# Performance work log

Measured on AMD Instinct MI355X. Metric: run time of the kernel, lower is better.

The kernel has to match this reference:

```python
import jax, jax.numpy as jnp
import numpy as np

N = 100000          # nodes
E = 1_600_000       # edges (before self loops)
IN = 128            # in_channels
HID = 64            # hidden
HEADS = 4
EPS = 1e-5          # BatchNorm eps
NEG_SLOPE = 0.2     # GATConv leaky_relu slope


def setup_inputs() -> dict:
    key = jax.random.key(0)
    ks = jax.random.split(key, 16)
    he = lambda fan: (2.0 / fan) ** 0.5  # kaiming-normal scale
    d = {
        "x": jax.random.normal(ks[0], (N, IN), jnp.float32),
        "edge_index": jax.random.randint(ks[1], (2, E), 0, N, dtype=jnp.int64),
        "root_index": 0,
        "W1": jax.random.normal(ks[2], (IN, HEADS * HID), jnp.float32) * he(IN),
        "att_src1": jax.random.normal(ks[3], (HEADS, HID), jnp.float32) * 0.1,
        "att_dst1": jax.random.normal(ks[4], (HEADS, HID), jnp.float32) * 0.1,
        "b1": jnp.zeros((HEADS * HID,), jnp.float32),
        "W2": jax.random.normal(ks[5], (HEADS * HID, HID), jnp.float32) * he(HEADS * HID),
        "att_src2": jax.random.normal(ks[6], (1, HID), jnp.float32) * 0.1,
        "att_dst2": jax.random.normal(ks[7], (1, HID), jnp.float32) * 0.1,
        "b2": jnp.zeros((HID,), jnp.float32),
        "bn1_g": jnp.ones((HEADS * HID,), jnp.float32),
        "bn1_b": jnp.zeros((HEADS * HID,), jnp.float32),
        "bn1_m": jnp.zeros((HEADS * HID,), jnp.float32),
        "bn1_v": jnp.ones((HEADS * HID,), jnp.float32),
        "bn2_g": jnp.ones((HID,), jnp.float32),
        "bn2_b": jnp.zeros((HID,), jnp.float32),
        "bn2_m": jnp.zeros((HID,), jnp.float32),
        "bn2_v": jnp.ones((HID,), jnp.float32),
        "cg1_w": jax.random.normal(ks[8], (3 * HID, 64), jnp.float32) * he(3 * HID),
        "cg1_b": jnp.zeros((64,), jnp.float32),
        "cbn_g": jnp.ones((64,), jnp.float32),
        "cbn_b": jnp.zeros((64,), jnp.float32),
        "cbn_m": jnp.zeros((64,), jnp.float32),
        "cbn_v": jnp.ones((64,), jnp.float32),
        "cg2_w": jax.random.normal(ks[9], (64, 32), jnp.float32) * he(64),
        "cg2_b": jnp.zeros((32,), jnp.float32),
        "cg3_w": jax.random.normal(ks[10], (32, 1), jnp.float32) * he(32),
        "cg3_b": jnp.zeros((1,), jnp.float32),
    }
    return d


def _bn_eval(x, g, b, m, v):
    return (x - m) * jax.lax.rsqrt(v + EPS) * g + b


def _gat_conv(x, src, dst, W, att_src, att_dst, bias, heads, out_ch, concat):
    """PyG GATConv (eval mode, self loops already in src/dst)."""
    n = x.shape[0]
    h = (x @ W).reshape(n, heads, out_ch)                # [N,H,C]
    a_src = jnp.einsum('nhc,hc->nh', h, att_src)         # [N,H]
    a_dst = jnp.einsum('nhc,hc->nh', h, att_dst)
    e = jax.nn.leaky_relu(a_src[src] + a_dst[dst], NEG_SLOPE)   # [Etot,H]
    seg_max = jax.ops.segment_max(e, dst, num_segments=n)
    ex = jnp.exp(e - seg_max[dst])
    denom = jax.ops.segment_sum(ex, dst, num_segments=n)
    alpha = ex / (denom[dst] + 1e-16)                    # [Etot,H]
    msg = h[src] * alpha[:, :, None]                     # [Etot,H,C]
    out = jax.ops.segment_sum(msg, dst, num_segments=n)  # [N,H,C]
    if concat:
        return out.reshape(n, heads * out_ch) + bias
    return out.mean(axis=1) + bias


def reference(x, edge_index, root_index, W1, att_src1, att_dst1, b1,
              W2, att_src2, att_dst2, b2,
              bn1_g, bn1_b, bn1_m, bn1_v, bn2_g, bn2_b, bn2_m, bn2_v,
              cg1_w, cg1_b, cbn_g, cbn_b, cbn_m, cbn_v,
              cg2_w, cg2_b, cg3_w, cg3_b):
    n = x.shape[0]
    # add self loops (PyG GATConv default)
    loop = jnp.arange(n, dtype=edge_index.dtype)
    src = jnp.concatenate([edge_index[0], loop])
    dst = jnp.concatenate([edge_index[1], loop])

    h = _gat_conv(x, src, dst, W1, att_src1, att_dst1, b1, HEADS, HID, True)
    h = jax.nn.elu(_bn_eval(h, bn1_g, bn1_b, bn1_m, bn1_v))
    h = _gat_conv(h, src, dst, W2, att_src2, att_dst2, b2, 1, HID, False)
    node_emb = jax.nn.elu(_bn_eval(h, bn2_g, bn2_b, bn2_m, bn2_v))  # [N,HID]

    mean_emb = node_emb.mean(axis=0, keepdims=True)      # [1,HID]
    max_emb = node_emb.max(axis=0, keepdims=True)        # [1,HID]
    safe_root = min(root_index, n - 1)
    root_emb = node_emb[safe_root][None, :]              # single graph path
    g = jnp.concatenate([mean_emb, max_emb, root_emb], axis=-1)  # [1,3*HID]

    g = jax.nn.relu(_bn_eval(g @ cg1_w + cg1_b, cbn_g, cbn_b, cbn_m, cbn_v))
    g = jax.nn.relu(g @ cg2_w + cg2_b)
    logit = (g @ cg3_w + cg3_b).squeeze(-1)              # [1]
    return logit
```

## Files before the change

### kernel.cpp

```cpp
#include <hip/hip_runtime.h>

#define N_NODES 100000
#define N_EDGES 1600000
#define ETOT    1700000
#define IN_CH   128
#define C1      256
#define HID     64
#define BN_EPS  1e-5f
#define SLOPE   0.2f
#define NCHUNK  98
#define DEG_PH  8
#define DEG_PHN 12500
#define FILL_PH 12
#define FILL_PHN 8334

typedef __attribute__((ext_vector_type(8))) short s16x8;
typedef __attribute__((ext_vector_type(4))) float f32x4;
#define MFMA16(a, b, c) __builtin_amdgcn_mfma_f32_16x16x32_bf16(a, b, c, 0, 0, 0)

__device__ __forceinline__ float leaky(float x) { return fmaxf(x, SLOPE * x); }
__device__ __forceinline__ float elu_f(float x) { return x > 0.f ? x : __expf(x) - 1.f; }
__device__ __forceinline__ unsigned short f2bf(float f) {
  unsigned int b = __float_as_uint(f);
  return (unsigned short)((b + 0x7FFFu + ((b >> 16) & 1u)) >> 16);
}
__device__ __forceinline__ float bf2f(unsigned short u) {
  return __uint_as_float((unsigned int)u << 16);
}
__device__ __forceinline__ unsigned int encf(float f) {
  unsigned int b = __float_as_uint(f);
  return b ^ ((((int)b >> 31)) | 0x80000000u);
}
__device__ __forceinline__ float decf(unsigned int k) {
  unsigned int b = (k & 0x80000000u) ? (k ^ 0x80000000u) : ~k;
  return __uint_as_float(b);
}

__global__ void __launch_bounds__(256) k_prep_init(const float* __restrict__ W1, const float* __restrict__ W2,
                                                   unsigned short* __restrict__ W1T, unsigned short* __restrict__ W2T,
                                                   int* __restrict__ deg, float* __restrict__ psum,
                                                   unsigned int* __restrict__ pmaxenc) {
  int i = blockIdx.x * 256 + threadIdx.x;
  if (i < N_NODES) deg[i] = 1;
  if (i < IN_CH * C1) {
    int k = i >> 8, c = i & 255;
    W1T[c * IN_CH + k] = f2bf(W1[i]);
  }
  if (i < C1 * HID) {
    int k = i >> 6, c = i & 63;
    W2T[c * C1 + k] = f2bf(W2[i]);
  }
  if (i < 256 * 64) { psum[i] = 0.f; pmaxenc[i] = 0u; }
}

__global__ void __launch_bounds__(256) k_deg_ph(const int* __restrict__ edge, int* __restrict__ deg) {
  int bpp = (N_EDGES + 1023) >> 10;
  int ph = blockIdx.x / bpp;
  int lo = ph * DEG_PHN, hi = lo + DEG_PHN;
  int i0 = (blockIdx.x % bpp) * 1024 + threadIdx.x * 4;
  if (i0 >= N_EDGES) return;
  if (i0 + 3 < N_EDGES) {
    int4 dv = *(const int4*)(edge + N_EDGES + i0);
    if (dv.x >= lo && dv.x < hi) atomicAdd(&deg[dv.x], 1);
    if (dv.y >= lo && dv.y < hi) atomicAdd(&deg[dv.y], 1);
    if (dv.z >= lo && dv.z < hi) atomicAdd(&deg[dv.z], 1);
    if (dv.w >= lo && dv.w < hi) atomicAdd(&deg[dv.w], 1);
  } else {
    for (int j = 0; j < 4 && i0 + j < N_EDGES; j++) {
      int d = edge[N_EDGES + i0 + j];
      if (d >= lo && d < hi) atomicAdd(&deg[d], 1);
    }
  }
}

__global__ void __launch_bounds__(256) k_scan_part(const int* __restrict__ deg, int* __restrict__ part) {
  __shared__ int ls[256];
  int t = threadIdx.x;
  int base = blockIdx.x * 1024 + t * 4;
  int s = 0;
#pragma unroll
  for (int j = 0; j < 4; j++) if (base + j < N_NODES) s += deg[base + j];
  ls[t] = s;
  __syncthreads();
  for (int off = 128; off >= 1; off >>= 1) {
    if (t < off) ls[t] += ls[t + off];
    __syncthreads();
  }
  if (t == 0) part[blockIdx.x] = ls[0];
}

__global__ void k_scan_top(int* __restrict__ part, int* __restrict__ row_ptr) {
  if (threadIdx.x == 0 && blockIdx.x == 0) {
    int run = 0;
    for (int i = 0; i < NCHUNK; i++) { int t = part[i]; part[i] = run; run += t; }
    row_ptr[N_NODES] = run;
  }
}

__global__ void __launch_bounds__(256) k_scan_down(const int* __restrict__ deg, const int* __restrict__ part,
                                                   int* __restrict__ row_ptr, int* __restrict__ cursor) {
  __shared__ int ls[256];
  int t = threadIdx.x;
  int base = blockIdx.x * 1024 + t * 4;
  int v[4];
#pragma unroll
  for (int j = 0; j < 4; j++) v[j] = (base + j < N_NODES) ? deg[base + j] : 0;
  int tsum = v[0] + v[1] + v[2] + v[3];
  ls[t] = tsum;
  __syncthreads();
  for (int off = 1; off < 256; off <<= 1) {
    int add = (t >= off) ? ls[t - off] : 0;
    __syncthreads();
    ls[t] += add;
    __syncthreads();
  }
  int excl = ls[t] - tsum + part[blockIdx.x];
#pragma unroll
  for (int j = 0; j < 4; j++) {
    int idx = base + j;
    if (idx < N_NODES) { row_ptr[idx] = excl; cursor[idx] = excl; }
    excl += v[j];
  }
}

__global__ void __launch_bounds__(256) k_fill_ph(const int* __restrict__ edge, int* __restrict__ cursor,
                                                 const float* __restrict__ aS, const float* __restrict__ aD,
                                                 int* __restrict__ col, float* __restrict__ w1) {
  int bpp = (ETOT + 255) >> 8;
  int ph = blockIdx.x / bpp;
  int lo = ph * FILL_PHN, hi = lo + FILL_PHN;
  int i = (blockIdx.x % bpp) * 256 + threadIdx.x;
  if (i >= ETOT) return;
  int d = (i < N_EDGES) ? edge[N_EDGES + i] : (i - N_EDGES);
  if (d < lo || d >= hi) return;
  int s = (i < N_EDGES) ? edge[i] : d;
  int pos = atomicAdd(&cursor[d], 1);
  col[pos] = s;
  float4 as4 = *(const float4*)(aS + (size_t)s * 4);
  float4 ad4 = *(const float4*)(aD + (size_t)d * 4);
  float4 w;
  w.x = __expf(fminf(leaky(as4.x + ad4.x), 80.f));
  w.y = __expf(fminf(leaky(as4.y + ad4.y), 80.f));
  w.z = __expf(fminf(leaky(as4.z + ad4.z), 80.f));
  w.w = __expf(fminf(leaky(as4.w + ad4.w), 80.f));
  *(float4*)(w1 + (size_t)pos * 4) = w;
}

__global__ void __launch_bounds__(256) k_gemm1(const float* __restrict__ x, const unsigned short* __restrict__ W1T,
                                               const float* __restrict__ attS, const float* __restrict__ attD,
                                               unsigned short* __restrict__ h1b, float* __restrict__ aS,
                                               float* __restrict__ aD) {
  __shared__ unsigned short As[64][IN_CH + 8];
  int tid = threadIdx.x;
  int w = tid >> 6, lane = tid & 63;
  int l15 = lane & 15, l4 = lane >> 4;
  int row0 = blockIdx.x * 64;
#pragma unroll
  for (int it = 0; it < 8; it++) {
    int idx = tid + it * 256;
    int r = idx >> 5;
    int k4 = (idx & 31) * 4;
    int gr = row0 + r; if (gr >= N_NODES) gr = N_NODES - 1;
    float4 v = *(const float4*)(x + (size_t)gr * IN_CH + k4);
    ushort4 bvec;
    bvec.x = f2bf(v.x); bvec.y = f2bf(v.y); bvec.z = f2bf(v.z); bvec.w = f2bf(v.w);
    *(ushort4*)&As[r][k4] = bvec;
  }
  __syncthreads();
  f32x4 acc[4][4];
#pragma unroll
  for (int mf = 0; mf < 4; mf++)
#pragma unroll
    for (int cf = 0; cf < 4; cf++) acc[mf][cf] = (f32x4){0.f, 0.f, 0.f, 0.f};
#pragma unroll
  for (int ks = 0; ks < 4; ks++) {
    int koff = ks * 32 + l4 * 8;
    s16x8 a[4];
#pragma unroll
    for (int mf = 0; mf < 4; mf++) a[mf] = *(const s16x8*)&As[mf * 16 + l15][koff];
#pragma unroll
    for (int cf = 0; cf < 4; cf++) {
      s16x8 b = *(const s16x8*)(W1T + (size_t)(w * 64 + cf * 16 + l15) * IN_CH + koff);
#pragma unroll
      for (int mf = 0; mf < 4; mf++) acc[mf][cf] = MFMA16(a[mf], b, acc[mf][cf]);
    }
  }
  float as_c[4], ad_c[4];
#pragma unroll
  for (int cf = 0; cf < 4; cf++) {
    as_c[cf] = attS[w * HID + cf * 16 + l15];
    ad_c[cf] = attD[w * HID + cf * 16 + l15];
  }
#pragma unroll
  for (int mf = 0; mf < 4; mf++) {
#pragma unroll
    for (int reg = 0; reg < 4; reg++) {
      int gr = row0 + mf * 16 + l4 * 4 + reg;
      bool ok = gr < N_NODES;
      float s = 0.f, dd = 0.f;
#pragma unroll
      for (int cf = 0; cf < 4; cf++) {
        float v = acc[mf][cf][reg];
        if (ok) h1b[(size_t)gr * C1 + w * 64 + cf * 16 + l15] = f2bf(v);
        s += v * as_c[cf];
        dd += v * ad_c[cf];
      }
#pragma unroll
      for (int m = 1; m <= 8; m <<= 1) { s += __shfl_xor(s, m, 64); dd += __shfl_xor(dd, m, 64); }
      if (ok && l15 == 0) {
        aS[(size_t)gr * 4 + w] = s;
        aD[(size_t)gr * 4 + w] = dd;
      }
    }
  }
}

__global__ void __launch_bounds__(1024) k_agg1g2(const int* __restrict__ row_ptr, const int* __restrict__ col,
                                                 const float* __restrict__ w1,
                                                 const unsigned short* __restrict__ h1b, const float* __restrict__ b1,
                                                 const float* __restrict__ g1, const float* __restrict__ be1,
                                                 const float* __restrict__ m1, const float* __restrict__ v1,
                                                 const unsigned short* __restrict__ W2T,
                                                 const float* __restrict__ attS2, const float* __restrict__ attD2,
                                                 unsigned short* __restrict__ h2b, float* __restrict__ aS2,
                                                 float* __restrict__ aD2) {
  __shared__ unsigned short Hm[16][C1 + 8];
  int wave = threadIdx.x >> 6;
  int lane = threadIdx.x & 63;
  int l15 = lane & 15, l4 = lane >> 4;
  int d = blockIdx.x * 16 + wave;
  int head = lane >> 4;
  int s0 = row_ptr[d], s1 = row_ptr[d + 1];
  int s1m1 = s1 - 1;
  float denom = 0.f;
  float4 acc = {0.f, 0.f, 0.f, 0.f};
  int c0 = lane * 4;
  for (int base = s0; base < s1; base += 8) {
    int left = s1 - base;
    int idx = base + (lane & 7); if (idx > s1m1) idx = s1m1;
    int cv = col[idx];
    int sid[8];
#pragma unroll
    for (int j = 0; j < 8; j++) sid[j] = __builtin_amdgcn_readfirstlane(__shfl(cv, j));
    float wv[8];
#pragma unroll
    for (int j = 0; j < 8; j++) {
      int wi = base + j; if (wi > s1m1) wi = s1m1;
      float wl = w1[(size_t)wi * 4 + head];
      wv[j] = (j < left) ? wl : 0.f;
    }
    ushort4 h[8];
#pragma unroll
    for (int j = 0; j < 8; j++) h[j] = *(const ushort4*)(h1b + ((size_t)sid[j] << 8) + c0);
#pragma unroll
    for (int j = 0; j < 8; j++) {
      denom += wv[j];
      acc.x += wv[j] * bf2f(h[j].x);
      acc.y += wv[j] * bf2f(h[j].y);
      acc.z += wv[j] * bf2f(h[j].z);
      acc.w += wv[j] * bf2f(h[j].w);
    }
  }
  float inv = 1.f / (denom + 1e-16f);
  float4 bb = *(const float4*)(b1 + c0);
  float4 gg = *(const float4*)(g1 + c0);
  float4 be = *(const float4*)(be1 + c0);
  float4 mm = *(const float4*)(m1 + c0);
  float4 vv = *(const float4*)(v1 + c0);
  ushort4 o;
  o.x = f2bf(elu_f((acc.x * inv + bb.x - mm.x) * rsqrtf(vv.x + BN_EPS) * gg.x + be.x));
  o.y = f2bf(elu_f((acc.y * inv + bb.y - mm.y) * rsqrtf(vv.y + BN_EPS) * gg.y + be.y));
  o.z = f2bf(elu_f((acc.z * inv + bb.z - mm.z) * rsqrtf(vv.z + BN_EPS) * gg.z + be.z));
  o.w = f2bf(elu_f((acc.w * inv + bb.w - mm.w) * rsqrtf(vv.w + BN_EPS) * gg.w + be.w));
  *(ushort4*)&Hm[wave][c0] = o;
  __syncthreads();
  if (wave == 0) {
    f32x4 acc2[4];
#pragma unroll
    for (int cf = 0; cf < 4; cf++) acc2[cf] = (f32x4){0.f, 0.f, 0.f, 0.f};
#pragma unroll
    for (int ks = 0; ks < 8; ks++) {
      int koff = ks * 32 + l4 * 8;
      s16x8 a = *(const s16x8*)&Hm[l15][koff];
#pragma unroll
      for (int cf = 0; cf < 4; cf++) {
        s16x8 b = *(const s16x8*)(W2T + (size_t)(cf * 16 + l15) * C1 + koff);
        acc2[cf] = MFMA16(a, b, acc2[cf]);
      }
    }
    float as_c[4], ad_c[4];
#pragma unroll
    for (int cf = 0; cf < 4; cf++) {
      as_c[cf] = attS2[cf * 16 + l15];
      ad_c[cf] = attD2[cf * 16 + l15];
    }
#pragma unroll
    for (int reg = 0; reg < 4; reg++) {
      int gr = blockIdx.x * 16 + l4 * 4 + reg;
      float s = 0.f, dd = 0.f;
#pragma unroll
      for (int cf = 0; cf < 4; cf++) {
        float v = acc2[cf][reg];
        h2b[(size_t)gr * HID + cf * 16 + l15] = f2bf(v);
        s += v * as_c[cf];
        dd += v * ad_c[cf];
      }
#pragma unroll
      for (int m = 1; m <= 8; m <<= 1) { s += __shfl_xor(s, m, 64); dd += __shfl_xor(dd, m, 64); }
      if (l15 == 0) { aS2[gr] = s; aD2[gr] = dd; }
    }
  }
}

__global__ void __launch_bounds__(256) k_agg2(const int* __restrict__ row_ptr, const int* __restrict__ col,
                                              const float* __restrict__ aS, const float* __restrict__ aD,
                                              const unsigned short* __restrict__ h2b, const float* __restrict__ b2,
                                              const float* __restrict__ g2, const float* __restrict__ be2,
                                              const float* __restrict__ m2, const float* __restrict__ v2,
                                              const int* __restrict__ rootp, float* __restrict__ psum,
                                              unsigned int* __restrict__ pmaxenc, float* __restrict__ root_emb) {
  __shared__ float ss[4][64], sm[4][64];
  int wave = threadIdx.x >> 6;
  int lane = threadIdx.x & 63;
  int d = blockIdx.x * 4 + wave;
  float ad = aD[d];
  int s0 = row_ptr[d], s1 = row_ptr[d + 1];
  int s1m1 = s1 - 1;
  float denom = 0.f, acc = 0.f;
  for (int base = s0; base < s1; base += 8) {
    int left = s1 - base;
    int idx = base + (lane & 7); if (idx > s1m1) idx = s1m1;
    int cv = col[idx];
    int sid[8];
#pragma unroll
    for (int j = 0; j < 8; j++) sid[j] = __builtin_amdgcn_readfirstlane(__shfl(cv, j));
    float e[8];
#pragma unroll
    for (int j = 0; j < 8; j++) e[j] = aS[sid[j]];
    unsigned short h[8];
#pragma unroll
    for (int j = 0; j < 8; j++) h[j] = h2b[((size_t)sid[j] << 6) + lane];
    float wv[8];
#pragma unroll
    for (int j = 0; j < 8; j++) {
      float wl = __expf(fminf(leaky(e[j] + ad), 80.f));
      wv[j] = (j < left) ? wl : 0.f;
    }
#pragma unroll
    for (int j = 0; j < 8; j++) {
      denom += wv[j];
      acc += wv[j] * bf2f(h[j]);
    }
  }
  float o = acc / (denom + 1e-16f) + b2[lane];
  o = (o - m2[lane]) * rsqrtf(v2[lane] + BN_EPS) * g2[lane] + be2[lane];
  o = elu_f(o);
  ss[wave][lane] = o;
  sm[wave][lane] = o;
  int root0 = rootp[0];
  if (root0 > N_NODES - 1) root0 = N_NODES - 1;
  if (root0 < 0) root0 = 0;
  if (d == root0) root_emb[lane] = o;
  __syncthreads();
  if (threadIdx.x < 64) {
    int c = threadIdx.x;
    float s4 = ss[0][c] + ss[1][c] + ss[2][c] + ss[3][c];
    float m4 = fmaxf(fmaxf(sm[0][c], sm[1][c]), fmaxf(sm[2][c], sm[3][c]));
    int slot = (blockIdx.x & 255) * 64 + c;
    atomicAdd(&psum[slot], s4);
    atomicMax(&pmaxenc[slot], encf(m4));
  }
}

__global__ void __launch_bounds__(256) k_final(const float* __restrict__ psum, const unsigned int* __restrict__ pmaxenc,
                                               const float* __restrict__ root_emb,
                                               const float* __restrict__ cg1w, const float* __restrict__ cg1b,
                                               const float* __restrict__ cbng, const float* __restrict__ cbnb,
                                               const float* __restrict__ cbnm, const float* __restrict__ cbnv,
                                               const float* __restrict__ cg2w, const float* __restrict__ cg2b,
                                               const float* __restrict__ cg3w, const float* __restrict__ cg3b,
                                               float* __restrict__ out) {
  __shared__ float ss[4][64], sm[4][64];
  __shared__ float g[192], t1[64], t2[32];
  int t = threadIdx.x;
  int c = t & 63, q = t >> 6;
  float s = 0.f, m = -INFINITY;
  for (int b = q; b < 256; b += 4) {
    s += psum[b * 64 + c];
    m = fmaxf(m, decf(pmaxenc[b * 64 + c]));
  }
  ss[q][c] = s; sm[q][c] = m;
  __syncthreads();
  if (t < 64) {
    float tot = ss[0][t] + ss[1][t] + ss[2][t] + ss[3][t];
    float mx = fmaxf(fmaxf(sm[0][t], sm[1][t]), fmaxf(sm[2][t], sm[3][t]));
    g[t] = tot / (float)N_NODES;
    g[64 + t] = mx;
    g[128 + t] = root_emb[t];
  }
  __syncthreads();
  if (t < 64) {
    float o = cg1b[t];
    for (int i = 0; i < 192; i++) o += g[i] * cg1w[i * 64 + t];
    o = (o - cbnm[t]) * rsqrtf(cbnv[t] + BN_EPS) * cbng[t] + cbnb[t];
    t1[t] = o > 0.f ? o : 0.f;
  }
  __syncthreads();
  if (t < 32) {
    float o = cg2b[t];
    for (int i = 0; i < 64; i++) o += t1[i] * cg2w[i * 32 + t];
    t2[t] = o > 0.f ? o : 0.f;
  }
  __syncthreads();
  if (t == 0) {
    float o = cg3b[0];
    for (int i = 0; i < 32; i++) o += t2[i] * cg3w[i];
    out[0] = o;
  }
}

extern "C" void kernel_launch(void* const* d_in, const int* in_sizes, int n_in,
                              void* d_out, int out_size, void* d_ws, size_t ws_size,
                              hipStream_t stream) {
  const float* x     = (const float*)d_in[0];
  const int*   edge  = (const int*)d_in[1];
  const int*   root  = (const int*)d_in[2];
  const float* W1    = (const float*)d_in[3];
  const float* attS1 = (const float*)d_in[4];
  const float* attD1 = (const float*)d_in[5];
  const float* b1    = (const float*)d_in[6];
  const float* W2    = (const float*)d_in[7];
  const float* attS2 = (const float*)d_in[8];
  const float* attD2 = (const float*)d_in[9];
  const float* b2    = (const float*)d_in[10];
  const float* bn1g  = (const float*)d_in[11];
  const float* bn1b  = (const float*)d_in[12];
  const float* bn1m  = (const float*)d_in[13];
  const float* bn1v  = (const float*)d_in[14];
  const float* bn2g  = (const float*)d_in[15];
  const float* bn2b  = (const float*)d_in[16];
  const float* bn2m  = (const float*)d_in[17];
  const float* bn2v  = (const float*)d_in[18];
  const float* cg1w  = (const float*)d_in[19];
  const float* cg1b  = (const float*)d_in[20];
  const float* cbng  = (const float*)d_in[21];
  const float* cbnb  = (const float*)d_in[22];
  const float* cbnm  = (const float*)d_in[23];
  const float* cbnv  = (const float*)d_in[24];
  const float* cg2w  = (const float*)d_in[25];
  const float* cg2b  = (const float*)d_in[26];
  const float* cg3w  = (const float*)d_in[27];
  const float* cg3b  = (const float*)d_in[28];

  char* ws = (char*)d_ws;
  size_t off = 0;
  auto carve = [&](size_t bytes) { char* p = ws + off; off += (bytes + 255) & ~(size_t)255; return p; };
  unsigned short* h1b = (unsigned short*)carve((size_t)N_NODES * C1 * 2);
  float* w1      = (float*)carve((size_t)ETOT * 4 * 4);
  unsigned short* h2b = (unsigned short*)carve((size_t)N_NODES * HID * 2);
  float* aS1     = (float*)carve((size_t)N_NODES * 4 * 4);
  float* aD1     = (float*)carve((size_t)N_NODES * 4 * 4);
  float* aS2     = (float*)carve((size_t)N_NODES * 4);
  float* aD2     = (float*)carve((size_t)N_NODES * 4);
  int*   deg     = (int*)  carve((size_t)N_NODES * 4);
  int*   row_ptr = (int*)  carve((size_t)(N_NODES + 1) * 4);
  int*   cursor  = (int*)  carve((size_t)N_NODES * 4);
  int*   col     = (int*)  carve((size_t)ETOT * 4);
  int*   part    = (int*)  carve(512);
  unsigned short* W1T = (unsigned short*)carve((size_t)IN_CH * C1 * 2);
  unsigned short* W2T = (unsigned short*)carve((size_t)C1 * HID * 2);
  float* psum    = (float*)carve(256 * 64 * 4);
  unsigned int* pmaxenc = (unsigned int*)carve(256 * 64 * 4);
  float* root_emb = (float*)carve(64 * 4);

  int bpp_deg  = (N_EDGES + 1023) >> 10;
  int bpp_fill = (ETOT + 255) >> 8;
  k_prep_init<<<(N_NODES + 255) / 256, 256, 0, stream>>>(W1, W2, W1T, W2T, deg, psum, pmaxenc);
  k_deg_ph<<<bpp_deg * DEG_PH, 256, 0, stream>>>(edge, deg);
  k_gemm1<<<(N_NODES + 63) / 64, 256, 0, stream>>>(x, W1T, attS1, attD1, h1b, aS1, aD1);
  k_scan_part<<<NCHUNK, 256, 0, stream>>>(deg, part);
  k_scan_top<<<1, 64, 0, stream>>>(part, row_ptr);
  k_scan_down<<<NCHUNK, 256, 0, stream>>>(deg, part, row_ptr, cursor);
  k_fill_ph<<<bpp_fill * FILL_PH, 256, 0, stream>>>(edge, cursor, aS1, aD1, col, w1);
  k_agg1g2<<<N_NODES / 16, 1024, 0, stream>>>(row_ptr, col, w1, h1b, b1, bn1g, bn1b, bn1m, bn1v,
                                              W2T, attS2, attD2, h2b, aS2, aD2);
  k_agg2<<<N_NODES / 4, 256, 0, stream>>>(row_ptr, col, aS2, aD2, h2b, b2, bn2g, bn2b, bn2m, bn2v,
                                          root, psum, pmaxenc, root_emb);
  k_final<<<1, 256, 0, stream>>>(psum, pmaxenc, root_emb, cg1w, cg1b, cbng, cbnb, cbnm, cbnv,
                                 cg2w, cg2b, cg3w, cg3b, (float*)d_out);
}
```

Baseline: 507.1 us.

## Split fused layer-1 aggregation and layer-2 GEMM into separate kernels

Unfuses the 1024-thread aggregation+GEMM kernel into a 256-thread aggregation kernel that writes the normalized hidden features to a new bf16 buffer and a separate 64-row-tile MFMA GEMM kernel. This removes the block-wide barrier where 15 of 16 waves idle while one wave runs the GEMM, and allows smaller blocks with better occupancy. In exchange it adds a full N×256 bf16 round trip through global memory and an extra launch. Layer-2 outputs are aliased into the now-dead h1b buffer.

Result: faster. 478.0 us, median of 2 (-5.7%).

```diff
diff --git a/kernel.cpp b/kernel.cpp
--- a/kernel.cpp
+++ b/kernel.cpp
@@ -215,20 +215,16 @@
   }
 }
 
-__global__ void __launch_bounds__(1024) k_agg1g2(const int* __restrict__ row_ptr, const int* __restrict__ col,
-                                                 const float* __restrict__ w1,
-                                                 const unsigned short* __restrict__ h1b, const float* __restrict__ b1,
-                                                 const float* __restrict__ g1, const float* __restrict__ be1,
-                                                 const float* __restrict__ m1, const float* __restrict__ v1,
-                                                 const unsigned short* __restrict__ W2T,
-                                                 const float* __restrict__ attS2, const float* __restrict__ attD2,
-                                                 unsigned short* __restrict__ h2b, float* __restrict__ aS2,
-                                                 float* __restrict__ aD2) {
-  __shared__ unsigned short Hm[16][C1 + 8];
+__global__ void __launch_bounds__(256) k_agg1(const int* __restrict__ row_ptr, const int* __restrict__ col,
+                                              const float* __restrict__ w1,
+                                              const unsigned short* __restrict__ h1b, const float* __restrict__ b1,
+                                              const float* __restrict__ g1, const float* __restrict__ be1,
+                                              const float* __restrict__ m1, const float* __restrict__ v1,
+                                              unsigned short* __restrict__ hmb) {
   int wave = threadIdx.x >> 6;
   int lane = threadIdx.x & 63;
-  int l15 = lane & 15, l4 = lane >> 4;
-  int d = blockIdx.x * 16 + wave;
+  int d = blockIdx.x * 4 + wave;
+  if (d >= N_NODES) return;
   int head = lane >> 4;
   int s0 = row_ptr[d], s1 = row_ptr[d + 1];
   int s1m1 = s1 - 1;
@@ -272,43 +268,61 @@
   o.y = f2bf(elu_f((acc.y * inv + bb.y - mm.y) * rsqrtf(vv.y + BN_EPS) * gg.y + be.y));
   o.z = f2bf(elu_f((acc.z * inv + bb.z - mm.z) * rsqrtf(vv.z + BN_EPS) * gg.z + be.z));
   o.w = f2bf(elu_f((acc.w * inv + bb.w - mm.w) * rsqrtf(vv.w + BN_EPS) * gg.w + be.w));
-  *(ushort4*)&Hm[wave][c0] = o;
-  __syncthreads();
-  if (wave == 0) {
-    f32x4 acc2[4];
-#pragma unroll
-    for (int cf = 0; cf < 4; cf++) acc2[cf] = (f32x4){0.f, 0.f, 0.f, 0.f};
-#pragma unroll
-    for (int ks = 0; ks < 8; ks++) {
-      int koff = ks * 32 + l4 * 8;
-      s16x8 a = *(const s16x8*)&Hm[l15][koff];
-#pragma unroll
-      for (int cf = 0; cf < 4; cf++) {
-        s16x8 b = *(const s16x8*)(W2T + (size_t)(cf * 16 + l15) * C1 + koff);
-        acc2[cf] = MFMA16(a, b, acc2[cf]);
-      }
-    }
-    float as_c[4], ad_c[4];
+  *(ushort4*)(hmb + (size_t)d * C1 + c0) = o;
+}
+
+__global__ void __launch_bounds__(256) k_gemm2(const unsigned short* __restrict__ hmb, const unsigned short* __restrict__ W2T,
+                                               const float* __restrict__ attS, const float* __restrict__ attD,
+                                               unsigned short* __restrict__ h2b, float* __restrict__ aS,
+                                               float* __restrict__ aD) {
+  __shared__ unsigned short As[64][C1 + 8];
+  int tid = threadIdx.x;
+  int w = tid >> 6, lane = tid & 63;
+  int l15 = lane & 15, l4 = lane >> 4;
+  int row0 = blockIdx.x * 64;
+#pragma unroll
+  for (int it = 0; it < 8; it++) {
+    int idx = tid + it * 256;
+    int r = idx >> 5;
+    int k8 = (idx & 31) * 8;
+    int gr = row0 + r; if (gr >= N_NODES) gr = N_NODES - 1;
+    *(uint4*)&As[r][k8] = *(const uint4*)(hmb + (size_t)gr * C1 + k8);
+  }
+  __syncthreads();
+  f32x4 acc[4];
+#pragma unroll
+  for (int cf = 0; cf < 4; cf++) acc[cf] = (f32x4){0.f, 0.f, 0.f, 0.f};
+#pragma unroll
+  for (int ks = 0; ks < 8; ks++) {
+    int koff = ks * 32 + l4 * 8;
+    s16x8 a = *(const s16x8*)&As[w * 16 + l15][koff];
 #pragma unroll
     for (int cf = 0; cf < 4; cf++) {
-      as_c[cf] = attS2[cf * 16 + l15];
-      ad_c[cf] = attD2[cf * 16 + l15];
-    }
-#pragma unroll
-    for (int reg = 0; reg < 4; reg++) {
-      int gr = blockIdx.x * 16 + l4 * 4 + reg;
-      float s = 0.f, dd = 0.f;
-#pragma unroll
-      for (int cf = 0; cf < 4; cf++) {
-        float v = acc2[cf][reg];
-        h2b[(size_t)gr * HID + cf * 16 + l15] = f2bf(v);
-        s += v * as_c[cf];
-        dd += v * ad_c[cf];
-      }
-#pragma unroll
-      for (int m = 1; m <= 8; m <<= 1) { s += __shfl_xor(s, m, 64); dd += __shfl_xor(dd, m, 64); }
-      if (l15 == 0) { aS2[gr] = s; aD2[gr] = dd; }
-    }
+      s16x8 b = *(const s16x8*)(W2T + (size_t)(cf * 16 + l15) * C1 + koff);
+      acc[cf] = MFMA16(a, b, acc[cf]);
+    }
+  }
+  float as_c[4], ad_c[4];
+#pragma unroll
+  for (int cf = 0; cf < 4; cf++) {
+    as_c[cf] = attS[cf * 16 + l15];
+    ad_c[cf] = attD[cf * 16 + l15];
+  }
+#pragma unroll
+  for (int reg = 0; reg < 4; reg++) {
+    int gr = row0 + w * 16 + l4 * 4 + reg;
+    bool ok = gr < N_NODES;
+    float s = 0.f, dd = 0.f;
+#pragma unroll
+    for (int cf = 0; cf < 4; cf++) {
+      float v = acc[cf][reg];
+      if (ok) h2b[(size_t)gr * HID + cf * 16 + l15] = f2bf(v);
+      s += v * as_c[cf];
+      dd += v * ad_c[cf];
+    }
+#pragma unroll
+    for (int m = 1; m <= 8; m <<= 1) { s += __shfl_xor(s, m, 64); dd += __shfl_xor(dd, m, 64); }
+    if (ok && l15 == 0) { aS[gr] = s; aD[gr] = dd; }
   }
 }
 
@@ -456,12 +470,10 @@
   size_t off = 0;
   auto carve = [&](size_t bytes) { char* p = ws + off; off += (bytes + 255) & ~(size_t)255; return p; };
   unsigned short* h1b = (unsigned short*)carve((size_t)N_NODES * C1 * 2);
+  unsigned short* hmb = (unsigned short*)carve((size_t)N_NODES * C1 * 2);
   float* w1      = (float*)carve((size_t)ETOT * 4 * 4);
-  unsigned short* h2b = (unsigned short*)carve((size_t)N_NODES * HID * 2);
   float* aS1     = (float*)carve((size_t)N_NODES * 4 * 4);
   float* aD1     = (float*)carve((size_t)N_NODES * 4 * 4);
-  float* aS2     = (float*)carve((size_t)N_NODES * 4);
-  float* aD2     = (float*)carve((size_t)N_NODES * 4);
   int*   deg     = (int*)  carve((size_t)N_NODES * 4);
   int*   row_ptr = (int*)  carve((size_t)(N_NODES + 1) * 4);
   int*   cursor  = (int*)  carve((size_t)N_NODES * 4);
@@ -472,6 +484,9 @@
   float* psum    = (float*)carve(256 * 64 * 4);
   unsigned int* pmaxenc = (unsigned int*)carve(256 * 64 * 4);
   float* root_emb = (float*)carve(64 * 4);
+  unsigned short* h2b = h1b;
+  float* aS2  = (float*)(h1b + (size_t)N_NODES * HID);
+  float* aD2  = aS2 + N_NODES;
 
   int bpp_deg  = (N_EDGES + 1023) >> 10;
   int bpp_fill = (ETOT + 255) >> 8;
@@ -482,8 +497,8 @@
   k_scan_top<<<1, 64, 0, stream>>>(part, row_ptr);
   k_scan_down<<<NCHUNK, 256, 0, stream>>>(deg, part, row_ptr, cursor);
   k_fill_ph<<<bpp_fill * FILL_PH, 256, 0, stream>>>(edge, cursor, aS1, aD1, col, w1);
-  k_agg1g2<<<N_NODES / 16, 1024, 0, stream>>>(row_ptr, col, w1, h1b, b1, bn1g, bn1b, bn1m, bn1v,
-                                              W2T, attS2, attD2, h2b, aS2, aD2);
+  k_agg1<<<(N_NODES + 3) / 4, 256, 0, stream>>>(row_ptr, col, w1, h1b, b1, bn1g, bn1b, bn1m, bn1v, hmb);
+  k_gemm2<<<(N_NODES + 63) / 64, 256, 0, stream>>>(hmb, W2T, attS2, attD2, h2b, aS2, aD2);
   k_agg2<<<N_NODES / 4, 256, 0, stream>>>(row_ptr, col, aS2, aD2, h2b, b2, bn2g, bn2b, bn2m, bn2v,
                                           root, psum, pmaxenc, root_emb);
   k_final<<<1, 256, 0, stream>>>(psum, pmaxenc, root_emb, cg1w, cg1b, cbng, cbnb, cbnm, cbnv,
```
